# Optimization experiments

Hardware: AMD Instinct MI355X
Metric: run time of the kernel (lower is better)

The kernel has to match this reference:

```python
import jax, jax.numpy as jnp
import numpy as np

# Model dims (Llama-7B-like GQA)
S, B, D_MODEL = 2048, 2, 4096   # total seq, batch, hidden
NH, NKV, HD = 32, 8, 128        # q heads, kv heads, head dim
TP = 4                          # ring size -> number of KV blocks
SB = S // TP                    # KV block length per ring step


def setup_inputs() -> dict:
    key = jax.random.key(0)
    k1, k2, k3 = jax.random.split(key, 3)
    hidden_states = jax.random.normal(k1, (S, B, D_MODEL), jnp.float32)
    w_qkv = jax.random.normal(k2, (D_MODEL, (NH + 2 * NKV) * HD), jnp.float32) / np.sqrt(D_MODEL)
    w_o = jax.random.normal(k3, (NH * HD, D_MODEL), jnp.float32) / np.sqrt(NH * HD)
    return {"hidden_states": hidden_states, "w_qkv": w_qkv, "w_o": w_o}


def _ring_attention(hidden_states, w_qkv, w_o):
    # fused QKV projection: [S,B,D] @ [D,(NH+2*NKV)*HD]
    qkv = hidden_states @ w_qkv
    q, k, v = jnp.split(qkv, [NH * HD, (NH + NKV) * HD], axis=-1)
    q = q.reshape(S, B, NH, HD).transpose(1, 2, 0, 3)    # [B,NH,S,HD]
    k = k.reshape(S, B, NKV, HD).transpose(1, 2, 0, 3)   # [B,NKV,S,HD]
    v = v.reshape(S, B, NKV, HD).transpose(1, 2, 0, 3)

    groups = NH // NKV  # GQA: expand kv heads to match q heads
    k = jnp.repeat(k, groups, axis=1)  # [B,NH,S,HD]
    v = jnp.repeat(v, groups, axis=1)

    scale = 1.0 / np.sqrt(HD)

    # Split K/V along sequence into TP ring blocks: [TP,B,NH,SB,HD]
    k_blocks = k.reshape(B, NH, TP, SB, HD).transpose(2, 0, 1, 3, 4)
    v_blocks = v.reshape(B, NH, TP, SB, HD).transpose(2, 0, 1, 3, 4)

    # Online-softmax (flash-attention style) accumulation over ring steps.
    m0 = jnp.full((B, NH, S), -jnp.inf, q.dtype)   # running row max
    l0 = jnp.zeros((B, NH, S), q.dtype)            # running denom
    acc0 = jnp.zeros((B, NH, S, HD), q.dtype)      # running numerator

    def step(carry, kv):
        m, l, acc = carry
        kb, vb = kv  # [B,NH,SB,HD]
        s = jnp.einsum('bhqd,bhkd->bhqk', q, kb) * scale  # [B,NH,S,SB]
        m_new = jnp.maximum(m, s.max(-1))
        p = jnp.exp(s - m_new[..., None])
        alpha = jnp.exp(m - m_new)
        l = l * alpha + p.sum(-1)
        acc = acc * alpha[..., None] + jnp.einsum('bhqk,bhkd->bhqd', p, vb)
        return (m_new, l, acc), None

    (m, l, acc), _ = jax.lax.scan(step, (m0, l0, acc0), (k_blocks, v_blocks))
    attn = acc / l[..., None]  # [B,NH,S,HD]

    # [B,NH,S,HD] -> [S*B, NH*HD] -> o_proj -> [S,B,D]
    attn = attn.transpose(2, 0, 1, 3).reshape(S * B, NH * HD)
    return (attn @ w_o).reshape(S, B, D_MODEL)


def reference(hidden_states, w_qkv, w_o):
    return _ring_attention(hidden_states, w_qkv, w_o)
```

## Files before the change

### kernel.cpp

```cpp
#include <hip/hip_runtime.h>
#include <hip/hip_bf16.h>


typedef __bf16 bf16x8 __attribute__((ext_vector_type(8)));
typedef float f32x4 __attribute__((ext_vector_type(4)));
typedef unsigned short u16;
typedef u16 u16x4 __attribute__((ext_vector_type(4)));
typedef u16 u16x8 __attribute__((ext_vector_type(8)));
typedef unsigned int u32;

#define SEQ    2048
#define BATCH  2
#define NROWS  4096
#define DM     4096
#define QKVC   6144
#define QSCALE (0.08838834764831845f * 1.4426950408889634f)

__device__ __forceinline__ u16 f2bf(float f) {
  union { float f; u32 u; } v; v.f = f;
  u32 r = v.u + 0x7fffu + ((v.u >> 16) & 1u);
  return (u16)(r >> 16);
}

__device__ __forceinline__ void gload16(const void* g, void* l) {
  __builtin_amdgcn_global_load_lds(
      (const __attribute__((address_space(1))) unsigned int*)g,
      (__attribute__((address_space(3))) unsigned int*)l, 16, 0, 0);
}

__global__ __launch_bounds__(256) void conv_f32_bf16(
    const float* __restrict__ in, u16* __restrict__ out) {
  size_t i = ((size_t)blockIdx.x * 256 + threadIdx.x) * 8;
  float4 a = *(const float4*)(in + i);
  float4 b = *(const float4*)(in + i + 4);
  u16x8 o;
  o[0] = f2bf(a.x); o[1] = f2bf(a.y); o[2] = f2bf(a.z); o[3] = f2bf(a.w);
  o[4] = f2bf(b.x); o[5] = f2bf(b.y); o[6] = f2bf(b.z); o[7] = f2bf(b.w);
  *(u16x8*)(out + i) = o;
}

__global__ __launch_bounds__(256) void transpose_f32_bf16(
    const float* __restrict__ in, u16* __restrict__ out, int K, int N) {
  __shared__ u16 tile[64][65];
  const int k0 = blockIdx.y * 64, n0 = blockIdx.x * 64;
  const int t = threadIdx.x;
#pragma unroll
  for (int i = 0; i < 4; ++i) {
    int slot = i * 256 + t;
    int r = slot >> 4, cq = slot & 15;
    float4 v = *(const float4*)(in + (size_t)(k0 + r) * N + n0 + cq * 4);
    tile[cq * 4 + 0][r] = f2bf(v.x);
    tile[cq * 4 + 1][r] = f2bf(v.y);
    tile[cq * 4 + 2][r] = f2bf(v.z);
    tile[cq * 4 + 3][r] = f2bf(v.w);
  }
  __syncthreads();
#pragma unroll
  for (int i = 0; i < 2; ++i) {
    int slot = i * 256 + t;
    int n = slot >> 3, q = slot & 7;
    u16x8 o;
#pragma unroll
    for (int e = 0; e < 8; ++e) o[e] = tile[n][q * 8 + e];
    *(u16x8*)(out + (size_t)(n0 + n) * K + k0 + q * 8) = o;
  }
}

__global__ __launch_bounds__(256) void vtrans(
    const u16* __restrict__ qkv, u16* __restrict__ vt) {
  __shared__ u16 tile[64][66];
  const int s0 = blockIdx.x * 64, d0 = blockIdx.y * 64;
  const int z = blockIdx.z;
  const int b = z >> 3, kvh = z & 7;
  const int t = threadIdx.x;
#pragma unroll
  for (int i = 0; i < 2; ++i) {
    int chunk = i * 256 + t;
    int r = chunk >> 3, q = chunk & 7;
    u16x8 v = *(const u16x8*)&qkv[(size_t)((s0 + r) * 2 + b) * QKVC + 5120 + kvh * 128 + d0 + q * 8];
#pragma unroll
    for (int e = 0; e < 8; ++e) tile[r][q * 8 + e] = v[e];
  }
  __syncthreads();
#pragma unroll
  for (int i = 0; i < 2; ++i) {
    int chunk = i * 256 + t;
    int d = chunk >> 3, q = chunk & 7;
    u16x8 o;
#pragma unroll
    for (int e = 0; e < 8; ++e) o[e] = tile[q * 8 + e][d];
    *(u16x8*)&vt[(size_t)(z * 128 + d0 + d) * SEQ + s0 + q * 8] = o;
  }
}

template <int CBF16, int SCALEQ>
__global__ __launch_bounds__(512, 2) void gemm192(
    const u16* __restrict__ A, const u16* __restrict__ B,
    void* __restrict__ C, int M, int N, int K, int nby) {
  __shared__ u16 As[2 * 16384];
  __shared__ u16 Bs[2 * 12288];
  const int t = threadIdx.x;
  const int w = t >> 6, l = t & 63;
  const int g = l >> 4, c = l & 15;
  const int wm = w >> 2, wn = w & 3;

  const int nwg = gridDim.x;
  const int sid = (blockIdx.x & 7) * (nwg >> 3) + (blockIdx.x >> 3);
  const int by = sid % nby, bx = sid / nby;
  const int m0 = by * 256, n0 = bx * 192;

  const int gsrc = (l & 7) ^ (l >> 3);
  const u16* pA = A + (size_t)(m0 + w * 8 + (l >> 3)) * K + gsrc * 8;
  const u16* pB = B + (size_t)(n0 + w * 8 + (l >> 3)) * K + gsrc * 8;

#define STG_A2(tt, hh) do { int d_ = (tt) & 1;                              \
    _Pragma("unroll")                                                       \
    for (int u = 0; u < 2; ++u)                                             \
      gload16(pA + (size_t)(((hh) * 2 + u) * 64) * K + (size_t)(tt) * 64,   \
              &As[d_ * 16384 + ((hh) * 2 + u) * 4096 + w * 512]); } while (0)
#define STG_B2(tt) do { int d_ = (tt) & 1;                                  \
    _Pragma("unroll")                                                       \
    for (int u = 0; u < 2; ++u)                                             \
      gload16(pB + (size_t)(u * 64) * K + (size_t)(tt) * 64,                \
              &Bs[d_ * 12288 + u * 4096 + w * 512]); } while (0)
#define STG_B1(tt) do { int d_ = (tt) & 1;                                  \
    gload16(pB + (size_t)(2 * 64) * K + (size_t)(tt) * 64,                  \
            &Bs[d_ * 12288 + 2 * 4096 + w * 512]); } while (0)

  const int xr0 = ((0 + g) ^ (c & 7)) << 3;
  const int xr1 = ((4 + g) ^ (c & 7)) << 3;

  const f32x4 fz = {0.f, 0.f, 0.f, 0.f};
  f32x4 acc[8][3];
#pragma unroll
  for (int m = 0; m < 8; ++m)
#pragma unroll
    for (int n = 0; n < 3; ++n) acc[m][n] = fz;

  const int nkt = K >> 6;
  STG_A2(0, 0); STG_A2(0, 1); STG_B2(0); STG_B1(0);
  STG_B2(1); STG_B1(1);
  asm volatile("s_waitcnt vmcnt(3)" ::: "memory");
  __builtin_amdgcn_sched_barrier(0);
  __builtin_amdgcn_s_barrier();

  for (int tt = 0; tt < nkt; ++tt) {
    const int d = tt & 1;
    const u16* aT = &As[d * 16384 + (wm * 128 + c) * 64];
    const u16* bT = &Bs[d * 12288 + (wn * 48 + c) * 64];
    bf16x8 a0[4], a1[4], bv[3][2];

#pragma unroll
    for (int m = 0; m < 4; ++m) a0[m] = *(const bf16x8*)(aT + m * 1024 + xr0);
#pragma unroll
    for (int n = 0; n < 3; ++n) bv[n][0] = *(const bf16x8*)(bT + n * 1024 + xr0);
    if (tt + 1 < nkt) STG_A2(tt + 1, 0);
    __builtin_amdgcn_s_barrier();
    __builtin_amdgcn_s_setprio(1);
#pragma unroll
    for (int m = 0; m < 4; ++m)
#pragma unroll
      for (int n = 0; n < 3; ++n)
        acc[m][n] = __builtin_amdgcn_mfma_f32_16x16x32_bf16(
            a0[m], bv[n][0], acc[m][n], 0, 0, 0);
    __builtin_amdgcn_s_setprio(0);
    __builtin_amdgcn_s_barrier();

#pragma unroll
    for (int m = 0; m < 4; ++m) a1[m] = *(const bf16x8*)(aT + m * 1024 + xr1);
#pragma unroll
    for (int n = 0; n < 3; ++n) bv[n][1] = *(const bf16x8*)(bT + n * 1024 + xr1);
    if (tt + 1 < nkt) STG_A2(tt + 1, 1);
    __builtin_amdgcn_s_barrier();
    __builtin_amdgcn_s_setprio(1);
#pragma unroll
    for (int m = 0; m < 4; ++m)
#pragma unroll
      for (int n = 0; n < 3; ++n)
        acc[m][n] = __builtin_amdgcn_mfma_f32_16x16x32_bf16(
            a1[m], bv[n][1], acc[m][n], 0, 0, 0);
    __builtin_amdgcn_s_setprio(0);
    __builtin_amdgcn_s_barrier();

#pragma unroll
    for (int m = 0; m < 4; ++m) a0[m] = *(const bf16x8*)(aT + (4 + m) * 1024 + xr0);
    if (tt + 2 < nkt) STG_B2(tt + 2);
    __builtin_amdgcn_s_barrier();
    __builtin_amdgcn_s_setprio(1);
#pragma unroll
    for (int m = 0; m < 4; ++m)
#pragma unroll
      for (int n = 0; n < 3; ++n)
        acc[4 + m][n] = __builtin_amdgcn_mfma_f32_16x16x32_bf16(
            a0[m], bv[n][0], acc[4 + m][n], 0, 0, 0);
    __builtin_amdgcn_s_setprio(0);
    __builtin_amdgcn_s_barrier();

#pragma unroll
    for (int m = 0; m < 4; ++m) a1[m] = *(const bf16x8*)(aT + (4 + m) * 1024 + xr1);
    if (tt + 2 < nkt) {
      STG_B1(tt + 2);
      asm volatile("s_waitcnt vmcnt(3)" ::: "memory");
    } else {
      asm volatile("s_waitcnt vmcnt(0)" ::: "memory");
    }
    __builtin_amdgcn_sched_barrier(0);
    __builtin_amdgcn_s_barrier();
    __builtin_amdgcn_s_setprio(1);
#pragma unroll
    for (int m = 0; m < 4; ++m)
#pragma unroll
      for (int n = 0; n < 3; ++n)
        acc[4 + m][n] = __builtin_amdgcn_mfma_f32_16x16x32_bf16(
            a1[m], bv[n][1], acc[4 + m][n], 0, 0, 0);
    __builtin_amdgcn_s_setprio(0);
    __builtin_amdgcn_s_barrier();
  }
#undef STG_A2
#undef STG_B2
#undef STG_B1

#pragma unroll
  for (int m = 0; m < 8; ++m)
#pragma unroll
    for (int n = 0; n < 3; ++n) {
      int row = m0 + wm * 128 + m * 16 + g * 4;
      int col = n0 + wn * 48 + n * 16 + c;
      float sc = (SCALEQ && col < 4096) ? QSCALE : 1.0f;
#pragma unroll
      for (int r = 0; r < 4; ++r) {
        float x = acc[m][n][r] * sc;
        if (CBF16) ((u16*)C)[(size_t)(row + r) * N + col] = f2bf(x);
        else       ((float*)C)[(size_t)(row + r) * N + col] = x;
      }
    }
}

template <int CBF16, int SCALEQ>
__global__ __launch_bounds__(512, 2) void gemm256(
    const u16* __restrict__ A, const u16* __restrict__ B,
    void* __restrict__ C, int M, int N, int K, int nby) {
  __shared__ u16 As[2 * 2 * 8192];
  __shared__ u16 Bs[2 * 2 * 8192];
  const int t = threadIdx.x;
  const int w = t >> 6, l = t & 63;
  const int g = l >> 4, c = l & 15;
  const int wm = w >> 2, wn = w & 3;

  const int nwg = gridDim.x;
  const int sid = (blockIdx.x & 7) * (nwg >> 3) + (blockIdx.x >> 3);
  const int by = sid % nby, bx = sid / nby;
  const int m0 = by * 256, n0 = bx * 256;

  const int gsrc = (l & 7) ^ (l >> 3);
  const u16* pA = A + (size_t)(m0 + w * 8 + (l >> 3)) * K + gsrc * 8;
  const u16* pB = B + (size_t)(n0 + w * 8 + (l >> 3)) * K + gsrc * 8;

#define STG_A(h, tt) do { int d_ = (tt) & 1;                                    \
    gload16(pA + (size_t)((h) * 128) * K + (tt) * 64,                           \
            &As[(d_ * 2 + (h)) * 8192 + w * 512]);                              \
    gload16(pA + (size_t)((h) * 128 + 64) * K + (tt) * 64,                      \
            &As[(d_ * 2 + (h)) * 8192 + 4096 + w * 512]); } while (0)
#define STG_B(h, tt) do { int d_ = (tt) & 1;                                    \
    gload16(pB + (size_t)((h) * 128) * K + (tt) * 64,                           \
            &Bs[(d_ * 2 + (h)) * 8192 + w * 512]);                              \
    gload16(pB + (size_t)((h) * 128 + 64) * K + (tt) * 64,                      \
            &Bs[(d_ * 2 + (h)) * 8192 + 4096 + w * 512]); } while (0)

  const u16* aRd = &As[wm * 8192 + c * 64];
  const u16* bRd = &Bs[(wn >> 1) * 8192 + ((wn & 1) * 64 + c) * 64];
  const int xr0 = ((0 + g) ^ (c & 7)) << 3;
  const int xr1 = ((4 + g) ^ (c & 7)) << 3;

  const f32x4 fz = {0.f, 0.f, 0.f, 0.f};
  f32x4 acc[8][4];
#pragma unroll
  for (int mi = 0; mi < 8; ++mi)
#pragma unroll
    for (int nj = 0; nj < 4; ++nj) acc[mi][nj] = fz;

  const int nkt = K >> 6;
  STG_A(0, 0); STG_A(1, 0); STG_B(0, 0); STG_B(1, 0);
  STG_B(0, 1); STG_B(1, 1);
  asm volatile("s_waitcnt vmcnt(4)" ::: "memory");
  __builtin_amdgcn_sched_barrier(0);
  __builtin_amdgcn_s_barrier();

  for (int tt = 0; tt < nkt; ++tt) {
    const int d = tt & 1;
    const u16* aT = aRd + d * 16384;
    const u16* bT = bRd + d * 16384;
    bf16x8 av[4][2], b01[2][2], b23[2][2];

#pragma unroll
    for (int m = 0; m < 4; ++m) {
      av[m][0] = *(const bf16x8*)(aT + m * 1024 + xr0);
      av[m][1] = *(const bf16x8*)(aT + m * 1024 + xr1);
    }
#pragma unroll
    for (int n = 0; n < 2; ++n) {
      b01[n][0] = *(const bf16x8*)(bT + n * 1024 + xr0);
      b01[n][1] = *(const bf16x8*)(bT + n * 1024 + xr1);
    }
    if (tt + 1 < nkt) STG_A(0, tt + 1);
    __builtin_amdgcn_s_barrier();
    __builtin_amdgcn_s_setprio(1);
#pragma unroll
    for (int kk = 0; kk < 2; ++kk)
#pragma unroll
      for (int m = 0; m < 4; ++m)
#pragma unroll
        for (int n = 0; n < 2; ++n)
          acc[m][n] = __builtin_amdgcn_mfma_f32_16x16x32_bf16(
              av[m][kk], b01[n][kk], acc[m][n], 0, 0, 0);
    __builtin_amdgcn_s_setprio(0);
    __builtin_amdgcn_s_barrier();

#pragma unroll
    for (int n = 0; n < 2; ++n) {
      b23[n][0] = *(const bf16x8*)(bT + (2 + n) * 1024 + xr0);
      b23[n][1] = *(const bf16x8*)(bT + (2 + n) * 1024 + xr1);
    }
    if (tt + 1 < nkt) STG_A(1, tt + 1);
    __builtin_amdgcn_s_barrier();
    __builtin_amdgcn_s_setprio(1);
#pragma unroll
    for (int kk = 0; kk < 2; ++kk)
#pragma unroll
      for (int m = 0; m < 4; ++m)
#pragma unroll
        for (int n = 0; n < 2; ++n)
          acc[m][2 + n] = __builtin_amdgcn_mfma_f32_16x16x32_bf16(
              av[m][kk], b23[n][kk], acc[m][2 + n], 0, 0, 0);
    __builtin_amdgcn_s_setprio(0);
    __builtin_amdgcn_s_barrier();

#pragma unroll
    for (int m = 0; m < 4; ++m) {
      av[m][0] = *(const bf16x8*)(aT + (4 + m) * 1024 + xr0);
      av[m][1] = *(const bf16x8*)(aT + (4 + m) * 1024 + xr1);
    }
    if (tt + 2 < nkt) STG_B(0, tt + 2);
    __builtin_amdgcn_s_barrier();
    __builtin_amdgcn_s_setprio(1);
#pragma unroll
    for (int kk = 0; kk < 2; ++kk)
#pragma unroll
      for (int m = 0; m < 4; ++m)
#pragma unroll
        for (int n = 0; n < 2; ++n)
          acc[4 + m][2 + n] = __builtin_amdgcn_mfma_f32_16x16x32_bf16(
              av[m][kk], b23[n][kk], acc[4 + m][2 + n], 0, 0, 0);
    __builtin_amdgcn_s_setprio(0);
    __builtin_amdgcn_s_barrier();

    if (tt + 2 < nkt) STG_B(1, tt + 2);
    if (tt < nkt - 2) asm volatile("s_waitcnt vmcnt(4)" ::: "memory");
    else              asm volatile("s_waitcnt vmcnt(0)" ::: "memory");
    __builtin_amdgcn_sched_barrier(0);
    __builtin_amdgcn_s_barrier();
    __builtin_amdgcn_s_setprio(1);
#pragma unroll
    for (int kk = 0; kk < 2; ++kk)
#pragma unroll
      for (int m = 0; m < 4; ++m)
#pragma unroll
        for (int n = 0; n < 2; ++n)
          acc[4 + m][n] = __builtin_amdgcn_mfma_f32_16x16x32_bf16(
              av[m][kk], b01[n][kk], acc[4 + m][n], 0, 0, 0);
    __builtin_amdgcn_s_setprio(0);
    __builtin_amdgcn_s_barrier();
  }
#undef STG_A
#undef STG_B

#pragma unroll
  for (int mi = 0; mi < 8; ++mi)
#pragma unroll
    for (int nj = 0; nj < 4; ++nj) {
      int row = m0 + wm * 128 + mi * 16 + g * 4;
      int col = n0 + wn * 64 + nj * 16 + c;
      float sc = (SCALEQ && col < 4096) ? QSCALE : 1.0f;
#pragma unroll
      for (int r = 0; r < 4; ++r) {
        float x = acc[mi][nj][r] * sc;
        if (CBF16) ((u16*)C)[(size_t)(row + r) * N + col] = f2bf(x);
        else       ((float*)C)[(size_t)(row + r) * N + col] = x;
      }
    }
}

__global__ __launch_bounds__(512, 4) void attn_fwd2(
    const u16* __restrict__ qkv, const u16* __restrict__ vtg,
    u16* __restrict__ out) {
  __shared__ u16 Ks[2][64 * 128];
  __shared__ u16 Vs[2][128 * 64];
  __shared__ u16 Ps[8][16 * 64];
  const int t = threadIdx.x;
  const int w = t >> 6, lane = t & 63;
  const int g = lane >> 4, c = lane & 15;
  const int bh = blockIdx.y;
  const int b = bh >> 5, h = bh & 31, kvh = h >> 2;
  const int q0 = blockIdx.x * 128 + w * 16;

  bf16x8 qf[4];
#pragma unroll
  for (int kk = 0; kk < 4; ++kk)
    qf[kk] = *(const bf16x8*)&qkv[(size_t)((q0 + c) * 2 + b) * QKVC + h * 128 + kk * 32 + g * 8];

  const f32x4 fz = {0.f, 0.f, 0.f, 0.f};
  f32x4 acc[8];
#pragma unroll
  for (int db = 0; db < 8; ++db) acc[db] = fz;
  float m_ = -__builtin_inff(), l_ = 0.f;

  const int w4g = w * 4 + g;
  const u16* pK = qkv + (size_t)b * QKVC + 4096 + kvh * 128 + (size_t)((c ^ w4g) & 15) * 8;
  const int vrow = w * 8 + (lane >> 3);
  const u16* pV = vtg + (size_t)(b * 8 + kvh) * 128 * SEQ + (size_t)((lane & 7) ^ (lane >> 3)) * 8;

  auto stage = [&](int bufi, int kv0) {
#pragma unroll
    for (int j = 0; j < 2; ++j)
      gload16(pK + (size_t)(kv0 + j * 32 + w4g) * (2 * QKVC), &Ks[bufi][(j * 8 + w) * 512]);
#pragma unroll
    for (int j = 0; j < 2; ++j)
      gload16(pV + (size_t)(j * 64 + vrow) * SEQ + kv0, &Vs[bufi][(j * 8 + w) * 512]);
  };

  stage(0, 0);
  int buf = 0;
  for (int kv0 = 0; kv0 < SEQ; kv0 += 64) {
    __syncthreads();
    if (kv0 + 64 < SEQ) stage(buf ^ 1, kv0 + 64);

    f32x4 st[4];
    __builtin_amdgcn_s_setprio(1);
#pragma unroll
    for (int kf = 0; kf < 4; ++kf) {
      const u16* kr = &Ks[buf][(kf * 16 + c) * 128];
      bf16x8 kfr[4];
#pragma unroll
      for (int kk = 0; kk < 4; ++kk)
        kfr[kk] = *(const bf16x8*)&kr[(((kk * 4 + g) ^ c) & 15) * 8];
      f32x4 s = fz;
#pragma unroll
      for (int kk = 0; kk < 4; ++kk)
        s = __builtin_amdgcn_mfma_f32_16x16x32_bf16(kfr[kk], qf[kk], s, 0, 0, 0);
      st[kf] = s;
    }
    __builtin_amdgcn_s_setprio(0);

    float mloc = st[0][0];
#pragma unroll
    for (int kf = 0; kf < 4; ++kf)
#pragma unroll
      for (int r = 0; r < 4; ++r) mloc = fmaxf(mloc, st[kf][r]);
    mloc = fmaxf(mloc, __shfl_xor(mloc, 16));
    mloc = fmaxf(mloc, __shfl_xor(mloc, 32));
    if (!__all(mloc - m_ <= 8.0f)) {
      float mnew = fmaxf(m_, mloc);
      float alpha = __builtin_amdgcn_exp2f(m_ - mnew);
      l_ *= alpha;
      f32x4 av;
#pragma unroll
      for (int r = 0; r < 4; ++r) av[r] = __shfl(alpha, g * 4 + r);
#pragma unroll
      for (int db = 0; db < 8; ++db) acc[db] *= av;
      m_ = mnew;
    }
    float ps = 0.f;
#pragma unroll
    for (int kf = 0; kf < 4; ++kf) {
      u16x4 pk;
#pragma unroll
      for (int r = 0; r < 4; ++r) {
        float p = __builtin_amdgcn_exp2f(st[kf][r] - m_);
        ps += p;
        pk[r] = f2bf(p);
      }
      *(u16x4*)&Ps[w][c * 64 + ((((kf * 2 + (g >> 1)) ^ (c & 7)) << 3) | ((g & 1) << 2))] = pk;
    }
    ps += __shfl_xor(ps, 16);
    ps += __shfl_xor(ps, 32);
    l_ += ps;

    bf16x8 pa0 = *(const bf16x8*)&Ps[w][c * 64 + (((0 + g) ^ (c & 7)) << 3)];
    bf16x8 pa1 = *(const bf16x8*)&Ps[w][c * 64 + (((4 + g) ^ (c & 7)) << 3)];
    __builtin_amdgcn_s_setprio(1);
#pragma unroll
    for (int db = 0; db < 8; ++db) {
      const u16* vr = &Vs[buf][(db * 16 + c) * 64];
      bf16x8 v0 = *(const bf16x8*)&vr[(((0 + g) ^ (c & 7)) << 3)];
      bf16x8 v1 = *(const bf16x8*)&vr[(((4 + g) ^ (c & 7)) << 3)];
      acc[db] = __builtin_amdgcn_mfma_f32_16x16x32_bf16(pa0, v0, acc[db], 0, 0, 0);
      acc[db] = __builtin_amdgcn_mfma_f32_16x16x32_bf16(pa1, v1, acc[db], 0, 0, 0);
    }
    __builtin_amdgcn_s_setprio(0);
    buf ^= 1;
  }

  float linv = __builtin_amdgcn_rcpf(l_);
  f32x4 il;
#pragma unroll
  for (int r = 0; r < 4; ++r) il[r] = __shfl(linv, g * 4 + r);
#pragma unroll
  for (int db = 0; db < 8; ++db) {
#pragma unroll
    for (int r = 0; r < 4; ++r) {
      int s = q0 + g * 4 + r;
      out[(size_t)(s * 2 + b) * DM + h * 128 + db * 16 + c] = f2bf(acc[db][r] * il[r]);
    }
  }
}

extern "C" void kernel_launch(void* const* d_in, const int* in_sizes, int n_in,
                              void* d_out, int out_size, void* d_ws, size_t ws_size,
                              hipStream_t stream) {
  const float* hidden = (const float*)d_in[0];
  const float* w_qkv  = (const float*)d_in[1];
  const float* w_o    = (const float*)d_in[2];
  float* outp = (float*)d_out;

  const size_t SZ_X  = (size_t)NROWS * DM * 2;
  const size_t SZ_WQ = (size_t)QKVC * DM * 2;
  const size_t SZ_WO = (size_t)DM * DM * 2;
  const size_t SZ_QKV = (size_t)NROWS * QKVC * 2;
  if (ws_size < SZ_X + SZ_WQ + SZ_WO + SZ_QKV) return;

  char* ws = (char*)d_ws;
  u16* Xb    = (u16*)ws;
  u16* WqkvT = (u16*)(ws + SZ_X);
  u16* WoT   = (u16*)(ws + SZ_X + SZ_WQ);
  u16* QKVb  = (u16*)(ws + SZ_X + SZ_WQ + SZ_WO);
  u16* VtG   = WqkvT;
  u16* Attn  = Xb;

  conv_f32_bf16<<<(NROWS * (size_t)DM) / 2048, 256, 0, stream>>>(hidden, Xb);
  transpose_f32_bf16<<<dim3(QKVC / 64, DM / 64), 256, 0, stream>>>(w_qkv, WqkvT, DM, QKVC);
  transpose_f32_bf16<<<dim3(DM / 64, DM / 64), 256, 0, stream>>>(w_o, WoT, DM, DM);
  gemm192<1, 1><<<512, 512, 0, stream>>>(Xb, WqkvT, QKVb, NROWS, QKVC, DM, 16);
  vtrans<<<dim3(SEQ / 64, 2, 16), 256, 0, stream>>>(QKVb, VtG);
  attn_fwd2<<<dim3(SEQ / 128, BATCH * 32), 512, 0, stream>>>(QKVb, VtG, Attn);
  gemm256<0, 0><<<256, 512, 0, stream>>>(Attn, WoT, outp, NROWS, DM, DM, 16);
}
```

Before: 554.6 us.

## Reorder GEMM main loop phases by B column group instead of K half

Restructures the four-phase MFMA inner loop of the QKV GEMM so each phase loads both K halves of the A fragments and iterates over B column groups, rather than splitting by K half. The B third column is loaded separately and the phases become cols 0-1 then col 2 for rows 0-3, then col 2 and cols 0-1 for rows 4-7. This changes how LDS reads interleave with the global-to-LDS staging and barriers, aiming for better overlap and fewer separate LDS reads of B. It raises register pressure by holding both K halves of A at once, and it changes when LDS data is read relative to the staging writes.

Result: no change. 554.7 us (+0.0%).

```diff
diff --git a/kernel.cpp b/kernel.cpp
--- a/kernel.cpp
+++ b/kernel.cpp
@@ -148,56 +148,63 @@
     const int d = tt & 1;
     const u16* aT = &As[d * 16384 + (wm * 128 + c) * 64];
     const u16* bT = &Bs[d * 12288 + (wn * 48 + c) * 64];
-    bf16x8 a0[4], a1[4], bv[3][2];
-
-#pragma unroll
-    for (int m = 0; m < 4; ++m) a0[m] = *(const bf16x8*)(aT + m * 1024 + xr0);
-#pragma unroll
-    for (int n = 0; n < 3; ++n) bv[n][0] = *(const bf16x8*)(bT + n * 1024 + xr0);
+    bf16x8 av[4][2], b01[2][2], b2[2];
+
+#pragma unroll
+    for (int m = 0; m < 4; ++m) {
+      av[m][0] = *(const bf16x8*)(aT + m * 1024 + xr0);
+      av[m][1] = *(const bf16x8*)(aT + m * 1024 + xr1);
+    }
+#pragma unroll
+    for (int n = 0; n < 2; ++n) {
+      b01[n][0] = *(const bf16x8*)(bT + n * 1024 + xr0);
+      b01[n][1] = *(const bf16x8*)(bT + n * 1024 + xr1);
+    }
     if (tt + 1 < nkt) STG_A2(tt + 1, 0);
     __builtin_amdgcn_s_barrier();
     __builtin_amdgcn_s_setprio(1);
 #pragma unroll
-    for (int m = 0; m < 4; ++m)
-#pragma unroll
-      for (int n = 0; n < 3; ++n)
-        acc[m][n] = __builtin_amdgcn_mfma_f32_16x16x32_bf16(
-            a0[m], bv[n][0], acc[m][n], 0, 0, 0);
-    __builtin_amdgcn_s_setprio(0);
-    __builtin_amdgcn_s_barrier();
-
-#pragma unroll
-    for (int m = 0; m < 4; ++m) a1[m] = *(const bf16x8*)(aT + m * 1024 + xr1);
-#pragma unroll
-    for (int n = 0; n < 3; ++n) bv[n][1] = *(const bf16x8*)(bT + n * 1024 + xr1);
+    for (int kk = 0; kk < 2; ++kk)
+#pragma unroll
+      for (int m = 0; m < 4; ++m)
+#pragma unroll
+        for (int n = 0; n < 2; ++n)
+          acc[m][n] = __builtin_amdgcn_mfma_f32_16x16x32_bf16(
+              av[m][kk], b01[n][kk], acc[m][n], 0, 0, 0);
+    __builtin_amdgcn_s_setprio(0);
+    __builtin_amdgcn_s_barrier();
+
+    b2[0] = *(const bf16x8*)(bT + 2 * 1024 + xr0);
+    b2[1] = *(const bf16x8*)(bT + 2 * 1024 + xr1);
     if (tt + 1 < nkt) STG_A2(tt + 1, 1);
     __builtin_amdgcn_s_barrier();
     __builtin_amdgcn_s_setprio(1);
 #pragma unroll
-    for (int m = 0; m < 4; ++m)
-#pragma unroll
-      for (int n = 0; n < 3; ++n)
-        acc[m][n] = __builtin_amdgcn_mfma_f32_16x16x32_bf16(
-            a1[m], bv[n][1], acc[m][n], 0, 0, 0);
-    __builtin_amdgcn_s_setprio(0);
-    __builtin_amdgcn_s_barrier();
-
-#pragma unroll
-    for (int m = 0; m < 4; ++m) a0[m] = *(const bf16x8*)(aT + (4 + m) * 1024 + xr0);
+    for (int kk = 0; kk < 2; ++kk)
+#pragma unroll
+      for (int m = 0; m < 4; ++m)
+        acc[m][2] = __builtin_amdgcn_mfma_f32_16x16x32_bf16(
+            av[m][kk], b2[kk], acc[m][2], 0, 0, 0);
+    __builtin_amdgcn_s_setprio(0);
+    __builtin_amdgcn_s_barrier();
+
+#pragma unroll
+    for (int m = 0; m < 4; ++m) {
+      av[m][0] = *(const bf16x8*)(aT + (4 + m) * 1024 + xr0);
+      av[m][1] = *(const bf16x8*)(aT + (4 + m) * 1024 + xr1);
+    }
     if (tt + 2 < nkt) STG_B2(tt + 2);
     __builtin_amdgcn_s_barrier();
     __builtin_amdgcn_s_setprio(1);
 #pragma unroll
-    for (int m = 0; m < 4; ++m)
-#pragma unroll
-      for (int n = 0; n < 3; ++n)
-        acc[4 + m][n] = __builtin_amdgcn_mfma_f32_16x16x32_bf16(
-            a0[m], bv[n][0], acc[4 + m][n], 0, 0, 0);
-    __builtin_amdgcn_s_setprio(0);
-    __builtin_amdgcn_s_barrier();
-
-#pragma unroll
-    for (int m = 0; m < 4; ++m) a1[m] = *(const bf16x8*)(aT + (4 + m) * 1024 + xr1);
+    for (int kk = 0; kk < 2; ++kk)
+#pragma unroll
+      for (int m = 0; m < 4; ++m)
+        acc[4 + m][2] = __builtin_amdgcn_mfma_f32_16x16x32_bf16(
+            av[m][kk], b2[kk], acc[4 + m][2], 0, 0, 0);
+    __builtin_amdgcn_s_setprio(0);
+    __builtin_amdgcn_s_barrier();
+
     if (tt + 2 < nkt) {
       STG_B1(tt + 2);
       asm volatile("s_waitcnt vmcnt(3)" ::: "memory");
@@ -208,11 +215,13 @@
     __builtin_amdgcn_s_barrier();
     __builtin_amdgcn_s_setprio(1);
 #pragma unroll
-    for (int m = 0; m < 4; ++m)
-#pragma unroll
-      for (int n = 0; n < 3; ++n)
-        acc[4 + m][n] = __builtin_amdgcn_mfma_f32_16x16x32_bf16(
-            a1[m], bv[n][1], acc[4 + m][n], 0, 0, 0);
+    for (int kk = 0; kk < 2; ++kk)
+#pragma unroll
+      for (int m = 0; m < 4; ++m)
+#pragma unroll
+        for (int n = 0; n < 2; ++n)
+          acc[4 + m][n] = __builtin_amdgcn_mfma_f32_16x16x32_bf16(
+              av[m][kk], b01[n][kk], acc[4 + m][n], 0, 0, 0);
     __builtin_amdgcn_s_setprio(0);
     __builtin_amdgcn_s_barrier();
   }
```
